# Optimization experiments

Measured on AMD Instinct MI355X. Metric: run time of the kernel, lower is better.

## Reference

```python
import jax, jax.numpy as jnp
import numpy as np

N_NODES = 50000
N_EDGES = 800000
D_IN = 128
HID = 128
N_CLASSES = 2
N_GRAPHS = 500
N_LAYERS = 7


def setup_inputs() -> dict:
    key = jax.random.key(0)
    ks = jax.random.split(key, 8)
    x = jax.random.normal(ks[0], (N_NODES, D_IN), dtype=jnp.float32)
    edge_index = jax.random.randint(ks[1], (2, N_EDGES), 0, N_NODES, dtype=jnp.int32)
    batch = jnp.sort(jax.random.randint(ks[2], (N_NODES,), 0, N_GRAPHS, dtype=jnp.int32))
    s = 1.0 / np.sqrt(HID).astype(np.float32)
    # SAGEConv params: Wl (neighbor lin, with bias bl), Wr (root lin, no bias)
    Wl = jax.random.normal(ks[3], (N_LAYERS, HID, HID), dtype=jnp.float32) * s
    Wr = jax.random.normal(ks[4], (N_LAYERS, HID, HID), dtype=jnp.float32) * s
    bl = jnp.zeros((N_LAYERS, HID), dtype=jnp.float32)
    W_out = jax.random.normal(ks[5], (HID, N_CLASSES), dtype=jnp.float32) * s
    b_out = jnp.zeros((N_CLASSES,), dtype=jnp.float32)
    return {"x": x, "edge_index": edge_index, "batch": batch,
            "Wl": Wl, "Wr": Wr, "bl": bl, "W_out": W_out, "b_out": b_out}


def reference(x, edge_index, batch, Wl, Wr, bl, W_out, b_out):
    n = x.shape[0]
    src, dst = edge_index[0], edge_index[1]  # messages flow src -> dst
    deg = jax.ops.segment_sum(jnp.ones_like(dst, dtype=x.dtype), dst, num_segments=n)
    inv_deg = (1.0 / jnp.clip(deg, 1.0))[:, None]  # [N,1]; zero-degree -> aggregate stays 0

    def sage_layer(h, i):
        # mean aggregation of neighbor features, then linear + root linear
        agg = jax.ops.segment_sum(h[src], dst, num_segments=n) * inv_deg  # [N,H]
        return agg @ Wl[i] + bl[i] + h @ Wr[i]

    h = x
    for i in range(N_LAYERS - 1):
        h = jax.nn.relu(sage_layer(h, i))
    h = sage_layer(h, N_LAYERS - 1)  # last conv: no relu

    pooled = jax.ops.segment_sum(h, batch, num_segments=N_GRAPHS)  # global_add_pool
    # F.dropout with training=False is identity (eval mode)
    return pooled @ W_out + b_out  # [G, num_classes]
```

## Files before the change

kernel.cpp:

```cpp
#include <hip/hip_runtime.h>
#include <stdint.h>

#define NN 50000
#define NE 800000
#define HID 128
#define NG 500
#define NL 7

typedef short bf16x8 __attribute__((ext_vector_type(8)));
typedef float f32x4 __attribute__((ext_vector_type(4)));

__device__ __forceinline__ unsigned short f2bf(float f) {
  unsigned int u = __builtin_bit_cast(unsigned int, f);
  u += 0x7FFFu + ((u >> 16) & 1u);
  return (unsigned short)(u >> 16);
}
__device__ __forceinline__ float bf2f(unsigned short h) {
  unsigned int u = ((unsigned int)h) << 16;
  return __builtin_bit_cast(float, u);
}
__device__ __forceinline__ float bflo(unsigned int u) {
  return __builtin_bit_cast(float, u << 16);
}
__device__ __forceinline__ float bfhi(unsigned int u) {
  return __builtin_bit_cast(float, u & 0xffff0000u);
}

__global__ void k_pre(const float* __restrict__ x, unsigned short* __restrict__ hA,
                      unsigned short* __restrict__ hB,
                      const int* __restrict__ dstE, int* __restrict__ deg,
                      const float* __restrict__ Wl, const float* __restrict__ Wr,
                      unsigned short* __restrict__ wswh,
                      unsigned short* __restrict__ wswl) {
  int i = blockIdx.x * 256 + threadIdx.x;
  if (i < NN * HID / 4) {
    float4 v = ((const float4*)x)[i];
    ushort4 r;
    r.x = f2bf(v.x); r.y = f2bf(v.y); r.z = f2bf(v.z); r.w = f2bf(v.w);
    ((ushort4*)hA)[i] = r;
  }
  if (i < NE) atomicAdd(&deg[dstE[i]], 1);
  if (i < NL * 2 * 4 * 4096) {
    int j = i & 7, ii = (i >> 3) & 15, q = (i >> 7) & 3, t = (i >> 9) & 7;
    int cc = (i >> 12) & 3, m = (i >> 14) & 1, l = i >> 15;
    int k = cc * 32 + q * 8 + j, n = t * 16 + ii;
    const float* W = m ? Wr : Wl;
    float w = W[l * HID * HID + k * HID + n];
    unsigned short hi = f2bf(w);
    unsigned short lo = f2bf(w - bf2f(hi));
    wswh[i] = hi;
    wswl[i] = lo;
  }
  if (i < 2048) {
    int b = i >> 10, r = (i >> 4) & 63, u = i & 15;
    unsigned short* pad = (b ? hB : hA) + (size_t)(NN + r) * HID;
    *(uint4*)&pad[u * 8] = make_uint4(0u, 0u, 0u, 0u);
  }
}

__global__ void k_scan1(const int* __restrict__ deg, int* __restrict__ offs,
                        int* __restrict__ bsum) {
  int i = blockIdx.x * 256 + threadIdx.x;
  int v = (i < NN) ? deg[i] : 0;
  int lane = threadIdx.x & 63, wv = threadIdx.x >> 6;
  int x = v;
  #pragma unroll
  for (int d = 1; d < 64; d <<= 1) {
    int y = __shfl_up(x, d, 64);
    if (lane >= d) x += y;
  }
  __shared__ int wsum[4];
  if (lane == 63) wsum[wv] = x;
  __syncthreads();
  if (threadIdx.x == 0) {
    int s = 0;
    for (int k = 0; k < 4; k++) { int t = wsum[k]; wsum[k] = s; s += t; }
    bsum[blockIdx.x] = s;
  }
  __syncthreads();
  if (i < NN) offs[i] = x - v + wsum[wv];
}

__global__ void k_scan2(int* __restrict__ bsum, int nb) {
  int i = threadIdx.x;
  int v = (i < nb) ? bsum[i] : 0;
  int lane = threadIdx.x & 63, wv = threadIdx.x >> 6;
  int x = v;
  #pragma unroll
  for (int d = 1; d < 64; d <<= 1) {
    int y = __shfl_up(x, d, 64);
    if (lane >= d) x += y;
  }
  __shared__ int wsum[4];
  if (lane == 63) wsum[wv] = x;
  __syncthreads();
  if (threadIdx.x == 0) {
    int s = 0;
    for (int k = 0; k < 4; k++) { int t = wsum[k]; wsum[k] = s; s += t; }
  }
  __syncthreads();
  if (i < nb) bsum[i] = x - v + wsum[wv];
}

__global__ void k_scan3(const int* __restrict__ deg, int* __restrict__ offs,
                        const int* __restrict__ bsum, float* __restrict__ invd) {
  int i = blockIdx.x * 256 + threadIdx.x;
  if (i < NN) {
    offs[i] += bsum[blockIdx.x];
    int d = deg[i];
    invd[i] = 1.0f / (float)(d > 0 ? d : 1);
    if (i == 0) offs[NN] = NE;
  }
}

#define FILL_CHUNK (NE / 128)
__global__ void k_fill(const int* __restrict__ src, const int* __restrict__ dst,
                       const int* __restrict__ offs, int* __restrict__ cur,
                       int* __restrict__ csr) {
  const int r = blockIdx.x & 7;
  const int chunk = blockIdx.x >> 3;
  const int lo = r * (NN / 8), hi = lo + (NN / 8);
  const int e0 = chunk * FILL_CHUNK;
  for (int e = e0 + threadIdx.x; e < e0 + FILL_CHUNK; e += 256) {
    int d = dst[e];
    if (d >= lo && d < hi) {
      int p = atomicAdd(&cur[d], 1);
      csr[offs[d] + p] = src[e];
    }
  }
}

#define ACC8(V) { a0 += bflo(V.x); a1 += bfhi(V.x); a2 += bflo(V.y); \
                  a3 += bfhi(V.y); a4 += bflo(V.z); a5 += bfhi(V.z); \
                  a6 += bflo(V.w); a7 += bfhi(V.w); }

#define LOADSTRIP(P0,P1,P2,P3,P4,P5,P6,P7,IDX) \
  P0 = *(const uint4*)(rowbase + (size_t)__shfl(IDX, 0, 8) * HID); \
  P1 = *(const uint4*)(rowbase + (size_t)__shfl(IDX, 1, 8) * HID); \
  P2 = *(const uint4*)(rowbase + (size_t)__shfl(IDX, 2, 8) * HID); \
  P3 = *(const uint4*)(rowbase + (size_t)__shfl(IDX, 3, 8) * HID); \
  P4 = *(const uint4*)(rowbase + (size_t)__shfl(IDX, 4, 8) * HID); \
  P5 = *(const uint4*)(rowbase + (size_t)__shfl(IDX, 5, 8) * HID); \
  P6 = *(const uint4*)(rowbase + (size_t)__shfl(IDX, 6, 8) * HID); \
  P7 = *(const uint4*)(rowbase + (size_t)__shfl(IDX, 7, 8) * HID);

__global__ __launch_bounds__(256, 6) void k_agg(const unsigned short* __restrict__ curh,
                                                const int* __restrict__ offs,
                                                const int* __restrict__ csr,
                                                const float* __restrict__ invd,
                                                unsigned short* __restrict__ agg) {
  const int g = blockIdx.x & 7;
  const int slice = g & 1;
  const int q = g >> 1;
  const int tid = threadIdx.x;
  const int grp = tid >> 3, l = tid & 7;
  const int local = (blockIdx.x >> 3) * 32 + grp;
  if (local >= NN / 4) return;
  const int node = q * (NN / 4) + local;
  const unsigned short* rowbase = curh + slice * 64 + l * 8;
  float a0 = 0.f, a1 = 0.f, a2 = 0.f, a3 = 0.f;
  float a4 = 0.f, a5 = 0.f, a6 = 0.f, a7 = 0.f;
  const int s = offs[node], e = offs[node + 1];
  if (s < e) {
    uint4 p0, p1, p2, p3, p4, p5, p6, p7;
    int idx = (s + l < e) ? csr[s + l] : NN;
    LOADSTRIP(p0, p1, p2, p3, p4, p5, p6, p7, idx)
    for (int base = s + 8; base < e; base += 8) {
      uint4 n0, n1, n2, n3, n4, n5, n6, n7;
      int idx2 = (base + l < e) ? csr[base + l] : NN;
      LOADSTRIP(n0, n1, n2, n3, n4, n5, n6, n7, idx2)
      ACC8(p0) ACC8(p1) ACC8(p2) ACC8(p3)
      ACC8(p4) ACC8(p5) ACC8(p6) ACC8(p7)
      p0 = n0; p1 = n1; p2 = n2; p3 = n3;
      p4 = n4; p5 = n5; p6 = n6; p7 = n7;
    }
    ACC8(p0) ACC8(p1) ACC8(p2) ACC8(p3)
    ACC8(p4) ACC8(p5) ACC8(p6) ACC8(p7)
  }
  float sc = invd[node];
  a0 *= sc; a1 *= sc; a2 *= sc; a3 *= sc;
  a4 *= sc; a5 *= sc; a6 *= sc; a7 *= sc;
  unsigned int w0 = (unsigned int)f2bf(a0) | ((unsigned int)f2bf(a1) << 16);
  unsigned int w1 = (unsigned int)f2bf(a2) | ((unsigned int)f2bf(a3) << 16);
  unsigned int w2 = (unsigned int)f2bf(a4) | ((unsigned int)f2bf(a5) << 16);
  unsigned int w3 = (unsigned int)f2bf(a6) | ((unsigned int)f2bf(a7) << 16);
  *(uint4*)(agg + (size_t)node * HID + slice * 64 + l * 8) =
      make_uint4(w0, w1, w2, w3);
}

__global__ __launch_bounds__(256) void k_gemm(const unsigned short* __restrict__ agg,
                                              const unsigned short* __restrict__ curh,
                                              const unsigned short* __restrict__ wswh,
                                              const unsigned short* __restrict__ wswl,
                                              const float* __restrict__ bias,
                                              unsigned short* __restrict__ out,
                                              int relu) {
  __shared__ __align__(16) unsigned short sW2[8192];
  const int tid = threadIdx.x;
  const int lane = tid & 63, wv = tid >> 6;
  const int row0 = blockIdx.x * 64;
  const int mr = (wv << 4) + (lane & 15);
  const int q = lane >> 4;
  const unsigned short* aRow = agg + (size_t)(row0 + mr) * HID + q * 8;
  const unsigned short* hRow = curh + (size_t)(row0 + mr) * HID + q * 8;

  f32x4 acc[8];
  #pragma unroll
  for (int t = 0; t < 8; t++) acc[t] = (f32x4){0.f, 0.f, 0.f, 0.f};

  for (int c = 0; c < 8; ++c) {
    const uint4* wh = (const uint4*)(wswh + c * 4096);
    const uint4* wl = (const uint4*)(wswl + c * 4096);
    ((uint4*)sW2)[tid] = wh[tid];
    ((uint4*)sW2)[tid + 256] = wh[tid + 256];
    ((uint4*)sW2)[tid + 512] = wl[tid];
    ((uint4*)sW2)[tid + 768] = wl[tid + 256];
    __syncthreads();
    bf16x8 a = *(const bf16x8*)(((c < 4) ? aRow : hRow) + (c & 3) * 32);
    #pragma unroll
    for (int t = 0; t < 8; t++) {
      bf16x8 bh = *(const bf16x8*)&sW2[(t * 4 + q) * 128 + (lane & 15) * 8];
      bf16x8 bl2 = *(const bf16x8*)&sW2[4096 + (t * 4 + q) * 128 + (lane & 15) * 8];
      acc[t] = __builtin_amdgcn_mfma_f32_16x16x32_bf16(a, bh, acc[t], 0, 0, 0);
      acc[t] = __builtin_amdgcn_mfma_f32_16x16x32_bf16(a, bl2, acc[t], 0, 0, 0);
    }
    __syncthreads();
  }

  const int ci = lane & 15;
  const int rb = (wv << 4) + (lane >> 4) * 4;
  #pragma unroll
  for (int t = 0; t < 8; t++) {
    int n = t * 16 + ci;
    float bn = bias[n];
    #pragma unroll
    for (int r2 = 0; r2 < 4; r2++) {
      int row = row0 + rb + r2;
      if (row < NN) {
        float v = acc[t][r2] + bn;
        if (relu) v = fmaxf(v, 0.f);
        out[(size_t)row * HID + n] = f2bf(v);
      }
    }
  }
}

__global__ void k_pool(const unsigned short* __restrict__ h,
                       const int* __restrict__ batch, float* __restrict__ pooled) {
  int g = blockIdx.x;
  __shared__ int rng[2];
  __shared__ float tmp[HID];
  if (threadIdx.x < 2) {
    int target = g + threadIdx.x;
    int lo = 0, hi = NN;
    while (lo < hi) {
      int mid = (lo + hi) >> 1;
      if (batch[mid] < target) lo = mid + 1; else hi = mid;
    }
    rng[threadIdx.x] = lo;
  }
  __syncthreads();
  int s = rng[0], e = rng[1];
  int f = threadIdx.x & 127, ro = threadIdx.x >> 7;
  float a = 0.f;
  for (int r = s + ro; r < e; r += 2) a += bf2f(h[(size_t)r * HID + f]);
  if (ro == 1) tmp[f] = a;
  __syncthreads();
  if (ro == 0) pooled[g * HID + f] = a + tmp[f];
}

__global__ void k_out(const float* __restrict__ pooled,
                      const float* __restrict__ Wout,
                      const float* __restrict__ bout,
                      float* __restrict__ out) {
  int g = blockIdx.x;
  int l = threadIdx.x;
  float a = pooled[g * HID + l], b = pooled[g * HID + 64 + l];
  float p0 = a * Wout[l * 2] + b * Wout[(l + 64) * 2];
  float p1 = a * Wout[l * 2 + 1] + b * Wout[(l + 64) * 2 + 1];
  #pragma unroll
  for (int d = 32; d; d >>= 1) {
    p0 += __shfl_down(p0, d, 64);
    p1 += __shfl_down(p1, d, 64);
  }
  if (l == 0) {
    out[g * 2] = p0 + bout[0];
    out[g * 2 + 1] = p1 + bout[1];
  }
}

extern "C" void kernel_launch(void* const* d_in, const int* in_sizes, int n_in,
                              void* d_out, int out_size, void* d_ws, size_t ws_size,
                              hipStream_t stream) {
  const float* x = (const float*)d_in[0];
  const int* ei = (const int*)d_in[1];
  const int* batch = (const int*)d_in[2];
  const float* Wl = (const float*)d_in[3];
  const float* Wr = (const float*)d_in[4];
  const float* bl = (const float*)d_in[5];
  const float* Wout = (const float*)d_in[6];
  const float* bout = (const float*)d_in[7];
  float* out = (float*)d_out;
  const int* srcE = ei;
  const int* dstE = ei + NE;

  char* w = (char*)d_ws;
  unsigned short* hA = (unsigned short*)w;  w += (size_t)(NN + 64) * HID * 2;
  unsigned short* hB = (unsigned short*)w;  w += (size_t)(NN + 64) * HID * 2;
  unsigned short* agg = (unsigned short*)w; w += (size_t)(NN + 64) * HID * 2;
  float* invd = (float*)w;   w += (size_t)NN * 4;
  float* pooled = (float*)w; w += (size_t)NG * HID * 4;
  int* deg = (int*)w;  w += (size_t)NN * 4;
  int* cur = (int*)w;  w += (size_t)NN * 4;
  int* offs = (int*)w; w += (size_t)50004 * 4;
  int* csr = (int*)w;  w += (size_t)NE * 4;
  int* bsum = (int*)w; w += 256 * 4;
  unsigned short* wswh = (unsigned short*)w; w += (size_t)NL * 2 * 4 * 4096 * 2;
  unsigned short* wswl = (unsigned short*)w;

  hipMemsetAsync(deg, 0, (size_t)NN * 2 * 4, stream);
  k_pre<<<(NN * HID / 4 + 255) / 256, 256, 0, stream>>>(x, hA, hB, dstE, deg,
                                                        Wl, Wr, wswh, wswl);
  int nb = (NN + 255) / 256;
  k_scan1<<<nb, 256, 0, stream>>>(deg, offs, bsum);
  k_scan2<<<1, 256, 0, stream>>>(bsum, nb);
  k_scan3<<<nb, 256, 0, stream>>>(deg, offs, bsum, invd);
  k_fill<<<1024, 256, 0, stream>>>(srcE, dstE, offs, cur, csr);

  unsigned short* curh = hA;
  unsigned short* nxth = hB;
  const int aggGrid = ((NN / 4 + 31) / 32) * 8;
  for (int l = 0; l < NL; l++) {
    k_agg<<<aggGrid, 256, 0, stream>>>(curh, offs, csr, invd, agg);
    k_gemm<<<(NN + 63) / 64, 256, 0, stream>>>(agg, curh,
                                               wswh + (size_t)l * 2 * 4 * 4096,
                                               wswl + (size_t)l * 2 * 4 * 4096,
                                               bl + l * HID, nxth,
                                               (l < NL - 1) ? 1 : 0);
    unsigned short* t = curh; curh = nxth; nxth = t;
  }
  k_pool<<<NG, 256, 0, stream>>>(curh, batch, pooled);
  k_out<<<NG, 64, 0, stream>>>(pooled, Wout, bout, out);
}
```

Baseline: 486.4 us.

## Bin nodes by degree for aggregation and double-buffer GEMM weight tiles

Adds a counting-sort pass that groups nodes into degree buckets and has the aggregation kernel process nodes in that permuted order, so the 32 node groups in a block see similar neighbor counts and idle less from imbalance. The previous quarter-based node partitioning is replaced by the permutation. Separately, the GEMM kernel now double-buffers the weight chunks in shared memory, prefetching the next chunk into registers while MFMAs run on the current one and removing one barrier per chunk. The cost is extra preprocessing kernels with atomics, loss of memory locality in the aggregation output writes, and more shared memory per GEMM block.

```diff
diff --git a/kernel.cpp b/kernel.cpp
--- a/kernel.cpp
+++ b/kernel.cpp
@@ -130,6 +130,29 @@
   }
 }
 
+__global__ void k_b1(const int* __restrict__ deg, int* __restrict__ bcnt) {
+  int i = blockIdx.x * 256 + threadIdx.x;
+  if (i < NN) {
+    int b = (deg[i] + 7) >> 3; if (b > 15) b = 15;
+    atomicAdd(&bcnt[b], 1);
+  }
+}
+__global__ void k_bscan(const int* __restrict__ bcnt, int* __restrict__ boff) {
+  if (threadIdx.x == 0) {
+    int s = 0;
+    for (int k = 0; k < 16; k++) { boff[k] = s; s += bcnt[k]; }
+  }
+}
+__global__ void k_b2(const int* __restrict__ deg, int* __restrict__ boff,
+                     int* __restrict__ perm) {
+  int i = blockIdx.x * 256 + threadIdx.x;
+  if (i < NN) {
+    int b = (deg[i] + 7) >> 3; if (b > 15) b = 15;
+    int p = atomicAdd(&boff[b], 1);
+    perm[p] = i;
+  }
+}
+
 #define ACC8(V) { a0 += bflo(V.x); a1 += bfhi(V.x); a2 += bflo(V.y); \
                   a3 += bfhi(V.y); a4 += bflo(V.z); a5 += bfhi(V.z); \
                   a6 += bflo(V.w); a7 += bfhi(V.w); }
@@ -148,15 +171,14 @@
                                                 const int* __restrict__ offs,
                                                 const int* __restrict__ csr,
                                                 const float* __restrict__ invd,
+                                                const int* __restrict__ perm,
                                                 unsigned short* __restrict__ agg) {
-  const int g = blockIdx.x & 7;
-  const int slice = g & 1;
-  const int q = g >> 1;
+  const int slice = blockIdx.x & 1;
   const int tid = threadIdx.x;
   const int grp = tid >> 3, l = tid & 7;
-  const int local = (blockIdx.x >> 3) * 32 + grp;
-  if (local >= NN / 4) return;
-  const int node = q * (NN / 4) + local;
+  const int pos = (blockIdx.x >> 1) * 32 + grp;
+  if (pos >= NN) return;
+  const int node = perm[pos];
   const unsigned short* rowbase = curh + slice * 64 + l * 8;
   float a0 = 0.f, a1 = 0.f, a2 = 0.f, a3 = 0.f;
   float a4 = 0.f, a5 = 0.f, a6 = 0.f, a7 = 0.f;
@@ -195,7 +217,7 @@
                                               const float* __restrict__ bias,
                                               unsigned short* __restrict__ out,
                                               int relu) {
-  __shared__ __align__(16) unsigned short sW2[8192];
+  __shared__ __align__(16) unsigned short sW2[2][8192];
   const int tid = threadIdx.x;
   const int lane = tid & 63, wv = tid >> 6;
   const int row0 = blockIdx.x * 64;
@@ -208,21 +230,38 @@
   #pragma unroll
   for (int t = 0; t < 8; t++) acc[t] = (f32x4){0.f, 0.f, 0.f, 0.f};
 
+  {
+    const uint4* wh = (const uint4*)wswh;
+    const uint4* wl = (const uint4*)wswl;
+    ((uint4*)sW2[0])[tid] = wh[tid];
+    ((uint4*)sW2[0])[tid + 256] = wh[tid + 256];
+    ((uint4*)sW2[0])[tid + 512] = wl[tid];
+    ((uint4*)sW2[0])[tid + 768] = wl[tid + 256];
+  }
+  __syncthreads();
+
   for (int c = 0; c < 8; ++c) {
-    const uint4* wh = (const uint4*)(wswh + c * 4096);
-    const uint4* wl = (const uint4*)(wswl + c * 4096);
-    ((uint4*)sW2)[tid] = wh[tid];
-    ((uint4*)sW2)[tid + 256] = wh[tid + 256];
-    ((uint4*)sW2)[tid + 512] = wl[tid];
-    ((uint4*)sW2)[tid + 768] = wl[tid + 256];
-    __syncthreads();
+    uint4 u0, u1, u2, u3;
+    if (c < 7) {
+      const uint4* wh = (const uint4*)(wswh + (c + 1) * 4096);
+      const uint4* wl = (const uint4*)(wswl + (c + 1) * 4096);
+      u0 = wh[tid]; u1 = wh[tid + 256]; u2 = wl[tid]; u3 = wl[tid + 256];
+    }
+    const unsigned short* buf = sW2[c & 1];
     bf16x8 a = *(const bf16x8*)(((c < 4) ? aRow : hRow) + (c & 3) * 32);
     #pragma unroll
     for (int t = 0; t < 8; t++) {
-      bf16x8 bh = *(const bf16x8*)&sW2[(t * 4 + q) * 128 + (lane & 15) * 8];
-      bf16x8 bl2 = *(const bf16x8*)&sW2[4096 + (t * 4 + q) * 128 + (lane & 15) * 8];
+      bf16x8 bh = *(const bf16x8*)&buf[(t * 4 + q) * 128 + (lane & 15) * 8];
+      bf16x8 bl2 = *(const bf16x8*)&buf[4096 + (t * 4 + q) * 128 + (lane & 15) * 8];
       acc[t] = __builtin_amdgcn_mfma_f32_16x16x32_bf16(a, bh, acc[t], 0, 0, 0);
       acc[t] = __builtin_amdgcn_mfma_f32_16x16x32_bf16(a, bl2, acc[t], 0, 0, 0);
+    }
+    if (c < 7) {
+      unsigned short* nb = sW2[(c + 1) & 1];
+      ((uint4*)nb)[tid] = u0;
+      ((uint4*)nb)[tid + 256] = u1;
+      ((uint4*)nb)[tid + 512] = u2;
+      ((uint4*)nb)[tid + 768] = u3;
     }
     __syncthreads();
   }
@@ -312,13 +351,16 @@
   float* pooled = (float*)w; w += (size_t)NG * HID * 4;
   int* deg = (int*)w;  w += (size_t)NN * 4;
   int* cur = (int*)w;  w += (size_t)NN * 4;
+  int* bcnt = (int*)w; w += 16 * 4;
+  int* boff = (int*)w; w += 16 * 4;
+  int* perm = (int*)w; w += (size_t)NN * 4;
   int* offs = (int*)w; w += (size_t)50004 * 4;
   int* csr = (int*)w;  w += (size_t)NE * 4;
   int* bsum = (int*)w; w += 256 * 4;
   unsigned short* wswh = (unsigned short*)w; w += (size_t)NL * 2 * 4 * 4096 * 2;
   unsigned short* wswl = (unsigned short*)w;
 
-  hipMemsetAsync(deg, 0, (size_t)NN * 2 * 4, stream);
+  hipMemsetAsync(deg, 0, ((size_t)NN * 2 + 16) * 4, stream);
   k_pre<<<(NN * HID / 4 + 255) / 256, 256, 0, stream>>>(x, hA, hB, dstE, deg,
                                                         Wl, Wr, wswh, wswl);
   int nb = (NN + 255) / 256;
@@ -326,12 +368,15 @@
   k_scan2<<<1, 256, 0, stream>>>(bsum, nb);
   k_scan3<<<nb, 256, 0, stream>>>(deg, offs, bsum, invd);
   k_fill<<<1024, 256, 0, stream>>>(srcE, dstE, offs, cur, csr);
+  k_b1<<<nb, 256, 0, stream>>>(deg, bcnt);
+  k_bscan<<<1, 64, 0, stream>>>(bcnt, boff);
+  k_b2<<<nb, 256, 0, stream>>>(deg, boff, perm);
 
   unsigned short* curh = hA;
   unsigned short* nxth = hB;
-  const int aggGrid = ((NN / 4 + 31) / 32) * 8;
+  const int aggGrid = ((NN + 31) / 32) * 2;
   for (int l = 0; l < NL; l++) {
-    k_agg<<<aggGrid, 256, 0, stream>>>(curh, offs, csr, invd, agg);
+    k_agg<<<aggGrid, 256, 0, stream>>>(curh, offs, csr, invd, perm, agg);
     k_gemm<<<(NN + 63) / 64, 256, 0, stream>>>(agg, curh,
                                                wswh + (size_t)l * 2 * 4 * 4096,
                                                wswl + (size_t)l * 2 * 4 * 4096,
```

After: 1.240 ms. +154.9%, slower.

## Reuse degree-count atomic ranks for CSR fill and double-buffer GEMM weight tiles

Applied to the files above, without the earlier changes.

The degree-counting atomic in the preprocessing kernel now stores its return value as a per-edge rank, so the CSR fill kernel writes each edge directly without a second atomic pass over a cursor array. Separately, the GEMM kernel double-buffers its shared-memory weight chunks: it prefetches the next chunk into registers while running MFMAs on the current one, which drops one barrier per chunk. The cost is an extra 3.2 MB rank array written and read back, plus twice the shared memory per GEMM block, which may lower occupancy.

```diff
diff --git a/kernel.cpp b/kernel.cpp
--- a/kernel.cpp
+++ b/kernel.cpp
@@ -29,6 +29,7 @@
 __global__ void k_pre(const float* __restrict__ x, unsigned short* __restrict__ hA,
                       unsigned short* __restrict__ hB,
                       const int* __restrict__ dstE, int* __restrict__ deg,
+                      int* __restrict__ rank,
                       const float* __restrict__ Wl, const float* __restrict__ Wr,
                       unsigned short* __restrict__ wswh,
                       unsigned short* __restrict__ wswl) {
@@ -39,7 +40,7 @@
     r.x = f2bf(v.x); r.y = f2bf(v.y); r.z = f2bf(v.z); r.w = f2bf(v.w);
     ((ushort4*)hA)[i] = r;
   }
-  if (i < NE) atomicAdd(&deg[dstE[i]], 1);
+  if (i < NE) rank[i] = atomicAdd(&deg[dstE[i]], 1);
   if (i < NL * 2 * 4 * 4096) {
     int j = i & 7, ii = (i >> 3) & 15, q = (i >> 7) & 3, t = (i >> 9) & 7;
     int cc = (i >> 12) & 3, m = (i >> 14) & 1, l = i >> 15;
@@ -115,7 +116,7 @@
 
 #define FILL_CHUNK (NE / 128)
 __global__ void k_fill(const int* __restrict__ src, const int* __restrict__ dst,
-                       const int* __restrict__ offs, int* __restrict__ cur,
+                       const int* __restrict__ rank, const int* __restrict__ offs,
                        int* __restrict__ csr) {
   const int r = blockIdx.x & 7;
   const int chunk = blockIdx.x >> 3;
@@ -123,10 +124,7 @@
   const int e0 = chunk * FILL_CHUNK;
   for (int e = e0 + threadIdx.x; e < e0 + FILL_CHUNK; e += 256) {
     int d = dst[e];
-    if (d >= lo && d < hi) {
-      int p = atomicAdd(&cur[d], 1);
-      csr[offs[d] + p] = src[e];
-    }
+    if (d >= lo && d < hi) csr[offs[d] + rank[e]] = src[e];
   }
 }
 
@@ -195,7 +193,7 @@
                                               const float* __restrict__ bias,
                                               unsigned short* __restrict__ out,
                                               int relu) {
-  __shared__ __align__(16) unsigned short sW2[8192];
+  __shared__ __align__(16) unsigned short sW2[2][8192];
   const int tid = threadIdx.x;
   const int lane = tid & 63, wv = tid >> 6;
   const int row0 = blockIdx.x * 64;
@@ -208,21 +206,38 @@
   #pragma unroll
   for (int t = 0; t < 8; t++) acc[t] = (f32x4){0.f, 0.f, 0.f, 0.f};
 
+  {
+    const uint4* wh = (const uint4*)wswh;
+    const uint4* wl = (const uint4*)wswl;
+    ((uint4*)sW2[0])[tid] = wh[tid];
+    ((uint4*)sW2[0])[tid + 256] = wh[tid + 256];
+    ((uint4*)sW2[0])[tid + 512] = wl[tid];
+    ((uint4*)sW2[0])[tid + 768] = wl[tid + 256];
+  }
+  __syncthreads();
+
   for (int c = 0; c < 8; ++c) {
-    const uint4* wh = (const uint4*)(wswh + c * 4096);
-    const uint4* wl = (const uint4*)(wswl + c * 4096);
-    ((uint4*)sW2)[tid] = wh[tid];
-    ((uint4*)sW2)[tid + 256] = wh[tid + 256];
-    ((uint4*)sW2)[tid + 512] = wl[tid];
-    ((uint4*)sW2)[tid + 768] = wl[tid + 256];
-    __syncthreads();
+    uint4 u0, u1, u2, u3;
+    if (c < 7) {
+      const uint4* wh = (const uint4*)(wswh + (c + 1) * 4096);
+      const uint4* wl = (const uint4*)(wswl + (c + 1) * 4096);
+      u0 = wh[tid]; u1 = wh[tid + 256]; u2 = wl[tid]; u3 = wl[tid + 256];
+    }
+    const unsigned short* buf = sW2[c & 1];
     bf16x8 a = *(const bf16x8*)(((c < 4) ? aRow : hRow) + (c & 3) * 32);
     #pragma unroll
     for (int t = 0; t < 8; t++) {
-      bf16x8 bh = *(const bf16x8*)&sW2[(t * 4 + q) * 128 + (lane & 15) * 8];
-      bf16x8 bl2 = *(const bf16x8*)&sW2[4096 + (t * 4 + q) * 128 + (lane & 15) * 8];
+      bf16x8 bh = *(const bf16x8*)&buf[(t * 4 + q) * 128 + (lane & 15) * 8];
+      bf16x8 bl2 = *(const bf16x8*)&buf[4096 + (t * 4 + q) * 128 + (lane & 15) * 8];
       acc[t] = __builtin_amdgcn_mfma_f32_16x16x32_bf16(a, bh, acc[t], 0, 0, 0);
       acc[t] = __builtin_amdgcn_mfma_f32_16x16x32_bf16(a, bl2, acc[t], 0, 0, 0);
+    }
+    if (c < 7) {
+      unsigned short* nb = sW2[(c + 1) & 1];
+      ((uint4*)nb)[tid] = u0;
+      ((uint4*)nb)[tid + 256] = u1;
+      ((uint4*)nb)[tid + 512] = u2;
+      ((uint4*)nb)[tid + 768] = u3;
     }
     __syncthreads();
   }
@@ -311,21 +326,21 @@
   float* invd = (float*)w;   w += (size_t)NN * 4;
   float* pooled = (float*)w; w += (size_t)NG * HID * 4;
   int* deg = (int*)w;  w += (size_t)NN * 4;
-  int* cur = (int*)w;  w += (size_t)NN * 4;
+  int* rank = (int*)w; w += (size_t)NE * 4;
   int* offs = (int*)w; w += (size_t)50004 * 4;
   int* csr = (int*)w;  w += (size_t)NE * 4;
   int* bsum = (int*)w; w += 256 * 4;
   unsigned short* wswh = (unsigned short*)w; w += (size_t)NL * 2 * 4 * 4096 * 2;
   unsigned short* wswl = (unsigned short*)w;
 
-  hipMemsetAsync(deg, 0, (size_t)NN * 2 * 4, stream);
+  hipMemsetAsync(deg, 0, (size_t)NN * 4, stream);
   k_pre<<<(NN * HID / 4 + 255) / 256, 256, 0, stream>>>(x, hA, hB, dstE, deg,
-                                                        Wl, Wr, wswh, wswl);
+                                                        rank, Wl, Wr, wswh, wswl);
   int nb = (NN + 255) / 256;
   k_scan1<<<nb, 256, 0, stream>>>(deg, offs, bsum);
   k_scan2<<<1, 256, 0, stream>>>(bsum, nb);
   k_scan3<<<nb, 256, 0, stream>>>(deg, offs, bsum, invd);
-  k_fill<<<1024, 256, 0, stream>>>(srcE, dstE, offs, cur, csr);
+  k_fill<<<1024, 256, 0, stream>>>(srcE, dstE, rank, offs, csr);
 
   unsigned short* curh = hA;
   unsigned short* nxth = hB;
```

After: 439.6 us (median of 2 runs). 1.11x faster.
